# Kernel optimization log

Hardware: AMD Instinct MI355X
Metric: run time of the kernel (lower is better)

Reference implementation:

```python
import jax, jax.numpy as jnp
import numpy as np

NUM_HEADS = 4
EPS = 1e-5


def setup_inputs() -> dict:
    key = jax.random.key(0)
    ks = jax.random.split(key, 5)
    B, C, H, W = 1, 128, 64, 64
    x = jax.random.normal(ks[0], (B, C, H, W), dtype=jnp.float32)
    # 1x1 conv weights [out_c, in_c]; scaled ~ kaiming-ish to keep softmax non-degenerate
    s = 1.0 / np.sqrt(C)
    qw = jax.random.normal(ks[1], (C, C), dtype=jnp.float32) * s
    kw = jax.random.normal(ks[2], (C, C), dtype=jnp.float32) * s
    vw = jax.random.normal(ks[3], (C, C), dtype=jnp.float32) * s
    pw = jax.random.normal(ks[4], (C, C), dtype=jnp.float32) * s
    zeros = jnp.zeros((C,), dtype=jnp.float32)
    return {
        "x": x,
        "gn_w": jnp.ones((C,), dtype=jnp.float32),
        "gn_b": zeros,
        "qw": qw, "qb": zeros,
        "kw": kw, "kb": zeros,
        "vw": vw, "vb": zeros,
        "pw": pw, "pb": zeros,
    }


def reference(x, gn_w, gn_b, qw, qb, kw, kb, vw, vb, pw, pb):
    B, C, H, W = x.shape
    N = H * W
    d = C // NUM_HEADS

    # GroupNorm(num_groups=1): normalize over (C,H,W) per sample, per-channel affine
    mean = jnp.mean(x, axis=(1, 2, 3), keepdims=True)
    var = jnp.var(x, axis=(1, 2, 3), keepdims=True)
    h = (x - mean) * jax.lax.rsqrt(var + EPS)
    h = h * gn_w[None, :, None, None] + gn_b[None, :, None, None]

    hf = h.reshape(B, C, N)  # [B,C,N]

    def conv1x1(w, b):  # 1x1 conv == channel GEMM
        return jnp.einsum('oc,bcn->bon', w, hf) + b[None, :, None]

    q = conv1x1(qw, qb).reshape(B, NUM_HEADS, d, N)
    k = conv1x1(kw, kb).reshape(B, NUM_HEADS, d, N)
    v = conv1x1(vw, vb).reshape(B, NUM_HEADS, d, N)

    scale = d ** (-0.5)
    attn = jnp.einsum('bhdn,bhdm->bhnm', q, k) * scale  # [B,H,N,N]
    attn = jax.nn.softmax(attn, axis=-1)
    out = jnp.einsum('bhnm,bhdm->bhdn', attn, v)  # [B,H,d,N]

    out = out.reshape(B, C, N)
    out = jnp.einsum('oc,bcn->bon', pw, out) + pb[None, :, None]
    return x + out.reshape(B, C, H, W)
```

## Files before the change

kernel.cpp:

```cpp
#include <hip/hip_runtime.h>

#define NPOS 4096
#define NCH  128
#define NTOT (NPOS * NCH)
#define NHEAD 4
#define DH    32
#define NSPLIT 4
#define KSPAN (NPOS / NSPLIT)

typedef __attribute__((ext_vector_type(8))) short short8;
typedef __attribute__((ext_vector_type(4))) float floatx4;
typedef unsigned short u16;
typedef unsigned int   u32;

__device__ __forceinline__ u16 f2bf(float f) {
  u32 u = __float_as_uint(f);
  u += 0x7fffu + ((u >> 16) & 1u);
  return (u16)(u >> 16);
}
__device__ __forceinline__ u32 pack2bf(float a, float b) {
  return (u32)f2bf(a) | ((u32)f2bf(b) << 16);
}
__device__ __forceinline__ u32 pack2bf_fast(float a, float b) {
  return ((__float_as_uint(a) + 0x8000u) >> 16) |
         ((__float_as_uint(b) + 0x8000u) & 0xffff0000u);
}
__device__ __forceinline__ float bf2f(u16 h) {
  return __uint_as_float(((u32)h) << 16);
}

__global__ __launch_bounds__(256) void gn_prep_k(const float* __restrict__ x,
                                                 float2* __restrict__ partials,
                                                 u32* __restrict__ bounds,
                                                 const float* __restrict__ qw, const float* __restrict__ kw,
                                                 const float* __restrict__ vw, const float* __restrict__ pw,
                                                 u16* __restrict__ wq, u16* __restrict__ wk,
                                                 u16* __restrict__ wv, u16* __restrict__ wp) {
  int i = blockIdx.x * 256 + threadIdx.x;
  int w = threadIdx.x >> 6, lane = threadIdx.x & 63;
  float4 a = ((const float4*)x)[i];
  float4 b = ((const float4*)x)[i + 65536];
  float s  = a.x + a.y + a.z + a.w + b.x + b.y + b.z + b.w;
  float sq = a.x*a.x + a.y*a.y + a.z*a.z + a.w*a.w
           + b.x*b.x + b.y*b.y + b.z*b.z + b.w*b.w;
#pragma unroll
  for (int m = 1; m < 64; m <<= 1) {
    s  += __shfl_xor(s, m);
    sq += __shfl_xor(sq, m);
  }
  __shared__ float red[8];
  if (lane == 0) { red[w] = s; red[4 + w] = sq; }
  __syncthreads();
  if (threadIdx.x == 0)
    partials[blockIdx.x] = make_float2(red[0]+red[1]+red[2]+red[3],
                                       red[4]+red[5]+red[6]+red[7]);
  if (blockIdx.x == 0 && threadIdx.x < 4) bounds[threadIdx.x] = 0;
  if (blockIdx.x < 16) {
    int t = blockIdx.x * 256 + threadIdx.x;
    const float sc = 0.17677669529663687f * 1.4426950408889634f;
    float4 v = ((const float4*)qw)[t];
    ((uint2*)wq)[t] = make_uint2(pack2bf(v.x*sc, v.y*sc), pack2bf(v.z*sc, v.w*sc));
    v = ((const float4*)kw)[t];
    ((uint2*)wk)[t] = make_uint2(pack2bf(v.x, v.y), pack2bf(v.z, v.w));
    v = ((const float4*)vw)[t];
    ((uint2*)wv)[t] = make_uint2(pack2bf(v.x, v.y), pack2bf(v.z, v.w));
    v = ((const float4*)pw)[t];
    ((uint2*)wp)[t] = make_uint2(pack2bf(v.x, v.y), pack2bf(v.z, v.w));
  }
}

__global__ __launch_bounds__(256) void qkv_k(const float* __restrict__ x,
    const float* __restrict__ gw, const float* __restrict__ gb,
    const float2* __restrict__ partials,
    const u16* __restrict__ wq, const u16* __restrict__ wk, const u16* __restrict__ wv,
    const float* __restrict__ qb, const float* __restrict__ kb, const float* __restrict__ vb,
    u16* __restrict__ q, u16* __restrict__ k, u16* __restrict__ v, u32* __restrict__ bounds) {
  const int t = threadIdx.x;
  const int w = t >> 6, lane = t & 63;
  const int l16 = lane & 15, quad = lane >> 4;
  const int n0 = blockIdx.x * 16, ow = w * 32;
  const floatx4 zero = {0.f, 0.f, 0.f, 0.f};

  __shared__ float red[8];
  __shared__ float2 swb[128];
  __shared__ __align__(16) u16 hs[16][136];

  float2 p = partials[t];
  float s = p.x, sq = p.y;
#pragma unroll
  for (int m = 1; m < 64; m <<= 1) {
    s  += __shfl_xor(s, m);
    sq += __shfl_xor(sq, m);
  }
  if (lane == 0) { red[w] = s; red[4 + w] = sq; }
  __syncthreads();
  float mean = (red[0]+red[1]+red[2]+red[3]) * (1.0f / NTOT);
  float var  = (red[4]+red[5]+red[6]+red[7]) * (1.0f / NTOT) - mean * mean;
  float rstd = rsqrtf(var + 1e-5f);
  if (t < 128) {
    float swv = gw[t] * rstd;
    swb[t] = make_float2(swv, gb[t] - mean * swv);
  }
  __syncthreads();

#pragma unroll
  for (int i = t; i < 512; i += 256) {
    int c = i >> 2, seg = i & 3;
    float4 xv = *(const float4*)(x + (size_t)c * NPOS + n0 + seg * 4);
    float2 sb = swb[c];
    int nl = seg * 4;
    hs[nl + 0][c] = f2bf(xv.x * sb.x + sb.y);
    hs[nl + 1][c] = f2bf(xv.y * sb.x + sb.y);
    hs[nl + 2][c] = f2bf(xv.z * sb.x + sb.y);
    hs[nl + 3][c] = f2bf(xv.w * sb.x + sb.y);
  }
  __syncthreads();

  short8 bfr[4];
#pragma unroll
  for (int kk = 0; kk < 4; kk++)
    bfr[kk] = *(const short8*)&hs[l16][kk * 32 + quad * 8];

  const int n = n0 + l16;
  {
    floatx4 a0 = zero, a1 = zero;
    const u16* ap = wq + (size_t)(ow + l16) * NCH + quad * 8;
#pragma unroll
    for (int kk = 0; kk < 4; kk++) {
      a0 = __builtin_amdgcn_mfma_f32_16x16x32_bf16(*(const short8*)(ap + kk*32),          bfr[kk], a0, 0,0,0);
      a1 = __builtin_amdgcn_mfma_f32_16x16x32_bf16(*(const short8*)(ap + 16*NCH + kk*32), bfr[kk], a1, 0,0,0);
    }
    const float sc = 0.17677669529663687f * 1.4426950408889634f;
    u16* qp = q + (size_t)(w * NPOS + n) * DH;
#pragma unroll
    for (int ss = 0; ss < 2; ss++) {
      floatx4 acc = ss ? a1 : a0;
      int od = ss * 16 + quad * 4;
      float r0 = acc[0] + qb[ow+od+0]*sc, r1 = acc[1] + qb[ow+od+1]*sc;
      float r2 = acc[2] + qb[ow+od+2]*sc, r3 = acc[3] + qb[ow+od+3]*sc;
      *(uint2*)(qp + od) = make_uint2(pack2bf(r0, r1), pack2bf(r2, r3));
    }
  }
  {
    floatx4 a0 = zero, a1 = zero;
    const u16* ap = wk + (size_t)(ow + l16) * NCH + quad * 8;
#pragma unroll
    for (int kk = 0; kk < 4; kk++) {
      a0 = __builtin_amdgcn_mfma_f32_16x16x32_bf16(*(const short8*)(ap + kk*32),          bfr[kk], a0, 0,0,0);
      a1 = __builtin_amdgcn_mfma_f32_16x16x32_bf16(*(const short8*)(ap + 16*NCH + kk*32), bfr[kk], a1, 0,0,0);
    }
    float sumsq = 0.f;
    u16* kp = k + (size_t)(w * NPOS + n) * DH;
#pragma unroll
    for (int ss = 0; ss < 2; ss++) {
      floatx4 acc = ss ? a1 : a0;
      int od = ss * 16 + quad * 4;
      float r0 = acc[0] + kb[ow+od+0], r1 = acc[1] + kb[ow+od+1];
      float r2 = acc[2] + kb[ow+od+2], r3 = acc[3] + kb[ow+od+3];
      sumsq += r0*r0 + r1*r1 + r2*r2 + r3*r3;
      *(uint2*)(kp + od) = make_uint2(pack2bf(r0, r1), pack2bf(r2, r3));
    }
    sumsq += __shfl_xor(sumsq, 16);
    sumsq += __shfl_xor(sumsq, 32);
#pragma unroll
    for (int m = 1; m < 16; m <<= 1) sumsq = fmaxf(sumsq, __shfl_xor(sumsq, m));
    if (lane == 0) atomicMax(&bounds[w], __float_as_uint(sumsq));
  }
  {
    floatx4 a0 = zero, a1 = zero;
    const u16* ap = wv + (size_t)(ow + l16) * NCH + quad * 8;
#pragma unroll
    for (int kk = 0; kk < 4; kk++) {
      a0 = __builtin_amdgcn_mfma_f32_16x16x32_bf16(*(const short8*)(ap + kk*32),          bfr[kk], a0, 0,0,0);
      a1 = __builtin_amdgcn_mfma_f32_16x16x32_bf16(*(const short8*)(ap + 16*NCH + kk*32), bfr[kk], a1, 0,0,0);
    }
    u16* vp = v + (size_t)(w * DH) * NPOS + n;
#pragma unroll
    for (int ss = 0; ss < 2; ss++) {
      floatx4 acc = ss ? a1 : a0;
      int od = ss * 16 + quad * 4;
#pragma unroll
      for (int r = 0; r < 4; r++)
        vp[(size_t)(od + r) * NPOS] = f2bf(acc[r] + vb[ow + od + r]);
    }
  }
}

__global__ __launch_bounds__(256) void attn_k(const u16* __restrict__ q, const u16* __restrict__ k,
                                              const u16* __restrict__ v, const u32* __restrict__ bounds,
                                              u32* __restrict__ Opair, float* __restrict__ lpart) {
  const int w = threadIdx.x >> 6, lane = threadIdx.x & 63;
  const int l16 = lane & 15, quad = lane >> 4;
  const int s = blockIdx.x >> 8;
  const int q0 = (blockIdx.x & 255) * 16;
  const int head = w;
  __shared__ __align__(16) u16 p_lds[4][2][16][72];

  short8 bq = *(const short8*)(q + (size_t)(head * NPOS + q0 + l16) * DH + quad * 8);
  float qn2 = 0.f;
#pragma unroll
  for (int j = 0; j < 8; j++) { float f = bf2f((u16)bq[j]); qn2 += f * f; }
  qn2 += __shfl_xor(qn2, 16);
  qn2 += __shfl_xor(qn2, 32);
  float kmax = sqrtf(__uint_as_float(bounds[head])) * 1.0005f;
  float bound = sqrtf(qn2) * kmax;

  floatx4 o0 = {0,0,0,0}, o1 = {0,0,0,0}, ol = {0,0,0,0};
  short8 ones;
#pragma unroll
  for (int j = 0; j < 8; j++) ones[j] = (short)0x3F80;

  const u16* kbp = k + (size_t)head * NPOS * DH;
  const u16* vb0 = v + (size_t)(head * DH + l16) * NPOS;
  const u16* vb1 = v + (size_t)(head * DH + 16 + l16) * NPOS;
  const floatx4 zero = {0,0,0,0};
  const int m0beg = s * KSPAN;

#pragma unroll 2
  for (int it = 0; it < KSPAN / 64; it++) {
    const int m0 = m0beg + it * 64;
    const int buf = it & 1;
    floatx4 c[4];
#pragma unroll
    for (int sub = 0; sub < 4; sub++) {
      short8 ak = *(const short8*)(kbp + (size_t)(m0 + sub*16 + l16) * DH + quad * 8);
      c[sub] = __builtin_amdgcn_mfma_f32_16x16x32_bf16(ak, bq, zero, 0, 0, 0);
    }
#pragma unroll
    for (int sub = 0; sub < 4; sub++) {
      float p0 = __builtin_amdgcn_exp2f(c[sub][0] - bound);
      float p1 = __builtin_amdgcn_exp2f(c[sub][1] - bound);
      float p2 = __builtin_amdgcn_exp2f(c[sub][2] - bound);
      float p3 = __builtin_amdgcn_exp2f(c[sub][3] - bound);
      *(uint2*)&p_lds[w][buf][l16][sub * 16 + quad * 4] =
          make_uint2(pack2bf_fast(p0, p1), pack2bf_fast(p2, p3));
    }
#pragma unroll
    for (int kc = 0; kc < 2; kc++) {
      short8 pa  = *(const short8*)&p_lds[w][buf][l16][kc * 32 + quad * 8];
      short8 av0 = *(const short8*)(vb0 + m0 + kc * 32 + quad * 8);
      short8 av1 = *(const short8*)(vb1 + m0 + kc * 32 + quad * 8);
      o0 = __builtin_amdgcn_mfma_f32_16x16x32_bf16(pa, av0, o0, 0, 0, 0);
      o1 = __builtin_amdgcn_mfma_f32_16x16x32_bf16(pa, av1, o1, 0, 0, 0);
      ol = __builtin_amdgcn_mfma_f32_16x16x32_bf16(pa, ones, ol, 0, 0, 0);
    }
  }

  u32*   op = Opair + (size_t)(s * NHEAD + head) * NPOS * 16;
  float* lp = lpart + (size_t)(s * NHEAD + head) * NPOS;
#pragma unroll
  for (int r = 0; r < 4; r++) {
    int qq = q0 + quad * 4 + r;
    op[(size_t)qq * 16 + l16] = pack2bf(o0[r], o1[r]);
    if (l16 == 0) lp[qq] = ol[r];
  }
}

__global__ __launch_bounds__(256) void proj_k(const u32* __restrict__ Opair,
                                              const float* __restrict__ lpart,
                                              const u16* __restrict__ wp,
                                              const float* __restrict__ pb,
                                              const float* __restrict__ x,
                                              float* __restrict__ out) {
  const int w = threadIdx.x >> 6, lane = threadIdx.x & 63;
  const int l16 = lane & 15, quad = lane >> 4;
  const int n0 = blockIdx.x * 16, ow = w * 32;
  const int n = n0 + l16;
  const floatx4 zero = {0.f, 0.f, 0.f, 0.f};
  const bool hi = quad >= 2;

  short8 bfr[4];
#pragma unroll
  for (int kk = 0; kk < 4; kk++) {
    float acc8[8] = {0,0,0,0,0,0,0,0};
    float l = 0.f;
#pragma unroll
    for (int s2 = 0; s2 < NSPLIT; s2++) {
      const u32* pp = Opair + ((size_t)(s2 * NHEAD + kk) * NPOS + n) * 16 + (quad & 1) * 8;
      uint4 u0 = *(const uint4*)pp;
      uint4 u1 = *(const uint4*)(pp + 4);
      u32 uu[8] = {u0.x, u0.y, u0.z, u0.w, u1.x, u1.y, u1.z, u1.w};
#pragma unroll
      for (int j = 0; j < 8; j++)
        acc8[j] += __uint_as_float(hi ? (uu[j] & 0xffff0000u) : (uu[j] << 16));
      l += lpart[(size_t)(s2 * NHEAD + kk) * NPOS + n];
    }
    float inv = 1.0f / fmaxf(l, 1e-30f);
    uint4 u = make_uint4(pack2bf(acc8[0]*inv, acc8[1]*inv),
                         pack2bf(acc8[2]*inv, acc8[3]*inv),
                         pack2bf(acc8[4]*inv, acc8[5]*inv),
                         pack2bf(acc8[6]*inv, acc8[7]*inv));
    bfr[kk] = *(short8*)&u;
  }
  floatx4 a0 = zero, a1 = zero;
  const u16* ap = wp + (size_t)(ow + l16) * NCH + quad * 8;
#pragma unroll
  for (int kk = 0; kk < 4; kk++) {
    a0 = __builtin_amdgcn_mfma_f32_16x16x32_bf16(*(const short8*)(ap + kk*32),          bfr[kk], a0, 0,0,0);
    a1 = __builtin_amdgcn_mfma_f32_16x16x32_bf16(*(const short8*)(ap + 16*NCH + kk*32), bfr[kk], a1, 0,0,0);
  }
#pragma unroll
  for (int ss = 0; ss < 2; ss++) {
    floatx4 acc = ss ? a1 : a0;
    int o = ow + ss * 16 + quad * 4;
#pragma unroll
    for (int r = 0; r < 4; r++) {
      size_t idx = (size_t)(o + r) * NPOS + n;
      out[idx] = acc[r] + pb[o + r] + x[idx];
    }
  }
}

extern "C" void kernel_launch(void* const* d_in, const int* in_sizes, int n_in,
                              void* d_out, int out_size, void* d_ws, size_t ws_size,
                              hipStream_t stream) {
  const float* x   = (const float*)d_in[0];
  const float* gnw = (const float*)d_in[1];
  const float* gnb = (const float*)d_in[2];
  const float* qw  = (const float*)d_in[3];
  const float* qb  = (const float*)d_in[4];
  const float* kw  = (const float*)d_in[5];
  const float* kb  = (const float*)d_in[6];
  const float* vw  = (const float*)d_in[7];
  const float* vb  = (const float*)d_in[8];
  const float* pw  = (const float*)d_in[9];
  const float* pb  = (const float*)d_in[10];
  float* out = (float*)d_out;

  char* wsb = (char*)d_ws;
  float2* partials = (float2*)wsb;
  u32*    bounds   = (u32*)(wsb + 2048);
  u16* wqb = (u16*)(wsb + 4096);
  u16* wkb = wqb + 16384;
  u16* wvb = wkb + 16384;
  u16* wpb = wvb + 16384;
  u16* qbuf = wpb + 16384;
  u16* kbuf = qbuf + NTOT;
  u16* vbuf = kbuf + NTOT;
  u32* Opair = (u32*)(vbuf + NTOT);
  float* lpart = (float*)(Opair + (size_t)NSPLIT * NHEAD * NPOS * 16);

  gn_prep_k<<<256, 256, 0, stream>>>(x, partials, bounds, qw, kw, vw, pw,
                                     wqb, wkb, wvb, wpb);
  qkv_k<<<256, 256, 0, stream>>>(x, gnw, gnb, partials, wqb, wkb, wvb,
                                 qb, kb, vb, qbuf, kbuf, vbuf, bounds);
  attn_k<<<1024, 256, 0, stream>>>(qbuf, kbuf, vbuf, bounds, Opair, lpart);
  proj_k<<<256, 256, 0, stream>>>(Opair, lpart, wpb, pb, x, out);
}
```

Before: 145.6 us.

## Widen per-block parallelism in prep/qkv/proj and register-prefetch K/V in attention

```diff
diff --git a/kernel.cpp b/kernel.cpp
--- a/kernel.cpp
+++ b/kernel.cpp
@@ -7,6 +7,7 @@
 #define DH    32
 #define NSPLIT 4
 #define KSPAN (NPOS / NSPLIT)
+#define NTILE (KSPAN / 64)
 
 typedef __attribute__((ext_vector_type(8))) short short8;
 typedef __attribute__((ext_vector_type(4))) float floatx4;
@@ -39,10 +40,8 @@
   int i = blockIdx.x * 256 + threadIdx.x;
   int w = threadIdx.x >> 6, lane = threadIdx.x & 63;
   float4 a = ((const float4*)x)[i];
-  float4 b = ((const float4*)x)[i + 65536];
-  float s  = a.x + a.y + a.z + a.w + b.x + b.y + b.z + b.w;
-  float sq = a.x*a.x + a.y*a.y + a.z*a.z + a.w*a.w
-           + b.x*b.x + b.y*b.y + b.z*b.z + b.w*b.w;
+  float s  = a.x + a.y + a.z + a.w;
+  float sq = a.x*a.x + a.y*a.y + a.z*a.z + a.w*a.w;
 #pragma unroll
   for (int m = 1; m < 64; m <<= 1) {
     s  += __shfl_xor(s, m);
@@ -69,7 +68,7 @@
   }
 }
 
-__global__ __launch_bounds__(256) void qkv_k(const float* __restrict__ x,
+__global__ __launch_bounds__(768) void qkv_k(const float* __restrict__ x,
     const float* __restrict__ gw, const float* __restrict__ gb,
     const float2* __restrict__ partials,
     const u16* __restrict__ wq, const u16* __restrict__ wk, const u16* __restrict__ wv,
@@ -78,34 +77,35 @@
   const int t = threadIdx.x;
   const int w = t >> 6, lane = t & 63;
   const int l16 = lane & 15, quad = lane >> 4;
-  const int n0 = blockIdx.x * 16, ow = w * 32;
+  const int n0 = blockIdx.x * 16;
   const floatx4 zero = {0.f, 0.f, 0.f, 0.f};
 
-  __shared__ float red[8];
+  __shared__ float red[16];
   __shared__ float2 swb[128];
   __shared__ __align__(16) u16 hs[16][136];
 
-  float2 p = partials[t];
-  float s = p.x, sq = p.y;
-#pragma unroll
-  for (int m = 1; m < 64; m <<= 1) {
-    s  += __shfl_xor(s, m);
-    sq += __shfl_xor(sq, m);
-  }
-  if (lane == 0) { red[w] = s; red[4 + w] = sq; }
-  __syncthreads();
-  float mean = (red[0]+red[1]+red[2]+red[3]) * (1.0f / NTOT);
-  float var  = (red[4]+red[5]+red[6]+red[7]) * (1.0f / NTOT) - mean * mean;
+  if (t < 512) {
+    float2 p = partials[t];
+    float s = p.x, sq = p.y;
+#pragma unroll
+    for (int m = 1; m < 64; m <<= 1) {
+      s  += __shfl_xor(s, m);
+      sq += __shfl_xor(sq, m);
+    }
+    if (lane == 0) { red[w] = s; red[8 + w] = sq; }
+  }
+  __syncthreads();
+  float mean = (red[0]+red[1]+red[2]+red[3]+red[4]+red[5]+red[6]+red[7]) * (1.0f / NTOT);
+  float var  = (red[8]+red[9]+red[10]+red[11]+red[12]+red[13]+red[14]+red[15]) * (1.0f / NTOT)
+               - mean * mean;
   float rstd = rsqrtf(var + 1e-5f);
   if (t < 128) {
     float swv = gw[t] * rstd;
     swb[t] = make_float2(swv, gb[t] - mean * swv);
   }
   __syncthreads();
-
-#pragma unroll
-  for (int i = t; i < 512; i += 256) {
-    int c = i >> 2, seg = i & 3;
+  if (t < 512) {
+    int c = t >> 2, seg = t & 3;
     float4 xv = *(const float4*)(x + (size_t)c * NPOS + n0 + seg * 4);
     float2 sb = swb[c];
     int nl = seg * 4;
@@ -121,17 +121,19 @@
   for (int kk = 0; kk < 4; kk++)
     bfr[kk] = *(const short8*)&hs[l16][kk * 32 + quad * 8];
 
+  const int mat = w >> 2, head = w & 3, ow = head * 32;
+  const u16* wm = (mat == 0) ? wq : (mat == 1) ? wk : wv;
+  floatx4 a0 = zero, a1 = zero;
+  const u16* ap = wm + (size_t)(ow + l16) * NCH + quad * 8;
+#pragma unroll
+  for (int kk = 0; kk < 4; kk++) {
+    a0 = __builtin_amdgcn_mfma_f32_16x16x32_bf16(*(const short8*)(ap + kk*32),          bfr[kk], a0, 0,0,0);
+    a1 = __builtin_amdgcn_mfma_f32_16x16x32_bf16(*(const short8*)(ap + 16*NCH + kk*32), bfr[kk], a1, 0,0,0);
+  }
   const int n = n0 + l16;
-  {
-    floatx4 a0 = zero, a1 = zero;
-    const u16* ap = wq + (size_t)(ow + l16) * NCH + quad * 8;
-#pragma unroll
-    for (int kk = 0; kk < 4; kk++) {
-      a0 = __builtin_amdgcn_mfma_f32_16x16x32_bf16(*(const short8*)(ap + kk*32),          bfr[kk], a0, 0,0,0);
-      a1 = __builtin_amdgcn_mfma_f32_16x16x32_bf16(*(const short8*)(ap + 16*NCH + kk*32), bfr[kk], a1, 0,0,0);
-    }
+  if (mat == 0) {
     const float sc = 0.17677669529663687f * 1.4426950408889634f;
-    u16* qp = q + (size_t)(w * NPOS + n) * DH;
+    u16* qp = q + (size_t)(head * NPOS + n) * DH;
 #pragma unroll
     for (int ss = 0; ss < 2; ss++) {
       floatx4 acc = ss ? a1 : a0;
@@ -140,17 +142,9 @@
       float r2 = acc[2] + qb[ow+od+2]*sc, r3 = acc[3] + qb[ow+od+3]*sc;
       *(uint2*)(qp + od) = make_uint2(pack2bf(r0, r1), pack2bf(r2, r3));
     }
-  }
-  {
-    floatx4 a0 = zero, a1 = zero;
-    const u16* ap = wk + (size_t)(ow + l16) * NCH + quad * 8;
-#pragma unroll
-    for (int kk = 0; kk < 4; kk++) {
-      a0 = __builtin_amdgcn_mfma_f32_16x16x32_bf16(*(const short8*)(ap + kk*32),          bfr[kk], a0, 0,0,0);
-      a1 = __builtin_amdgcn_mfma_f32_16x16x32_bf16(*(const short8*)(ap + 16*NCH + kk*32), bfr[kk], a1, 0,0,0);
-    }
+  } else if (mat == 1) {
     float sumsq = 0.f;
-    u16* kp = k + (size_t)(w * NPOS + n) * DH;
+    u16* kp = k + (size_t)(head * NPOS + n) * DH;
 #pragma unroll
     for (int ss = 0; ss < 2; ss++) {
       floatx4 acc = ss ? a1 : a0;
@@ -164,17 +158,9 @@
     sumsq += __shfl_xor(sumsq, 32);
 #pragma unroll
     for (int m = 1; m < 16; m <<= 1) sumsq = fmaxf(sumsq, __shfl_xor(sumsq, m));
-    if (lane == 0) atomicMax(&bounds[w], __float_as_uint(sumsq));
-  }
-  {
-    floatx4 a0 = zero, a1 = zero;
-    const u16* ap = wv + (size_t)(ow + l16) * NCH + quad * 8;
-#pragma unroll
-    for (int kk = 0; kk < 4; kk++) {
-      a0 = __builtin_amdgcn_mfma_f32_16x16x32_bf16(*(const short8*)(ap + kk*32),          bfr[kk], a0, 0,0,0);
-      a1 = __builtin_amdgcn_mfma_f32_16x16x32_bf16(*(const short8*)(ap + 16*NCH + kk*32), bfr[kk], a1, 0,0,0);
-    }
-    u16* vp = v + (size_t)(w * DH) * NPOS + n;
+    if (lane == 0) atomicMax(&bounds[head], __float_as_uint(sumsq));
+  } else {
+    u16* vp = v + (size_t)(head * DH) * NPOS + n;
 #pragma unroll
     for (int ss = 0; ss < 2; ss++) {
       floatx4 acc = ss ? a1 : a0;
@@ -210,22 +196,41 @@
 #pragma unroll
   for (int j = 0; j < 8; j++) ones[j] = (short)0x3F80;
 
-  const u16* kbp = k + (size_t)head * NPOS * DH;
-  const u16* vb0 = v + (size_t)(head * DH + l16) * NPOS;
-  const u16* vb1 = v + (size_t)(head * DH + 16 + l16) * NPOS;
+  const u16* kbp = k + (size_t)head * NPOS * DH + quad * 8;
+  const u16* vb0 = v + (size_t)(head * DH + l16) * NPOS + quad * 8;
+  const u16* vb1 = vb0 + (size_t)16 * NPOS;
   const floatx4 zero = {0,0,0,0};
-  const int m0beg = s * KSPAN;
-
-#pragma unroll 2
-  for (int it = 0; it < KSPAN / 64; it++) {
-    const int m0 = m0beg + it * 64;
+
+  int m0 = s * KSPAN;
+  short8 ak[4], av[4];
+#pragma unroll
+  for (int sub = 0; sub < 4; sub++)
+    ak[sub] = *(const short8*)(kbp + (size_t)(m0 + sub * 16 + l16) * DH);
+#pragma unroll
+  for (int kc = 0; kc < 2; kc++) {
+    av[2*kc]   = *(const short8*)(vb0 + m0 + kc * 32);
+    av[2*kc+1] = *(const short8*)(vb1 + m0 + kc * 32);
+  }
+
+  for (int it = 0; it < NTILE; it++) {
+    const int mn = m0 + 64;
+    const bool more = (it + 1 < NTILE);
+    short8 nak[4], nav[4];
+    if (more) {
+#pragma unroll
+      for (int sub = 0; sub < 4; sub++)
+        nak[sub] = *(const short8*)(kbp + (size_t)(mn + sub * 16 + l16) * DH);
+#pragma unroll
+      for (int kc = 0; kc < 2; kc++) {
+        nav[2*kc]   = *(const short8*)(vb0 + mn + kc * 32);
+        nav[2*kc+1] = *(const short8*)(vb1 + mn + kc * 32);
+      }
+    }
     const int buf = it & 1;
     floatx4 c[4];
 #pragma unroll
-    for (int sub = 0; sub < 4; sub++) {
-      short8 ak = *(const short8*)(kbp + (size_t)(m0 + sub*16 + l16) * DH + quad * 8);
-      c[sub] = __builtin_amdgcn_mfma_f32_16x16x32_bf16(ak, bq, zero, 0, 0, 0);
-    }
+    for (int sub = 0; sub < 4; sub++)
+      c[sub] = __builtin_amdgcn_mfma_f32_16x16x32_bf16(ak[sub], bq, zero, 0, 0, 0);
 #pragma unroll
     for (int sub = 0; sub < 4; sub++) {
       float p0 = __builtin_amdgcn_exp2f(c[sub][0] - bound);
@@ -237,13 +242,16 @@
     }
 #pragma unroll
     for (int kc = 0; kc < 2; kc++) {
-      short8 pa  = *(const short8*)&p_lds[w][buf][l16][kc * 32 + quad * 8];
-      short8 av0 = *(const short8*)(vb0 + m0 + kc * 32 + quad * 8);
-      short8 av1 = *(const short8*)(vb1 + m0 + kc * 32 + quad * 8);
-      o0 = __builtin_amdgcn_mfma_f32_16x16x32_bf16(pa, av0, o0, 0, 0, 0);
-      o1 = __builtin_amdgcn_mfma_f32_16x16x32_bf16(pa, av1, o1, 0, 0, 0);
-      ol = __builtin_amdgcn_mfma_f32_16x16x32_bf16(pa, ones, ol, 0, 0, 0);
-    }
+      short8 pa = *(const short8*)&p_lds[w][buf][l16][kc * 32 + quad * 8];
+      o0 = __builtin_amdgcn_mfma_f32_16x16x32_bf16(pa, av[2*kc],   o0, 0, 0, 0);
+      o1 = __builtin_amdgcn_mfma_f32_16x16x32_bf16(pa, av[2*kc+1], o1, 0, 0, 0);
+      ol = __builtin_amdgcn_mfma_f32_16x16x32_bf16(pa, ones,       ol, 0, 0, 0);
+    }
+    if (more) {
+#pragma unroll
+      for (int j = 0; j < 4; j++) { ak[j] = nak[j]; av[j] = nav[j]; }
+    }
+    m0 = mn;
   }
 
   u32*   op = Opair + (size_t)(s * NHEAD + head) * NPOS * 16;
@@ -256,58 +264,58 @@
   }
 }
 
-__global__ __launch_bounds__(256) void proj_k(const u32* __restrict__ Opair,
+__global__ __launch_bounds__(512) void proj_k(const u32* __restrict__ Opair,
                                               const float* __restrict__ lpart,
                                               const u16* __restrict__ wp,
                                               const float* __restrict__ pb,
                                               const float* __restrict__ x,
                                               float* __restrict__ out) {
-  const int w = threadIdx.x >> 6, lane = threadIdx.x & 63;
+  const int t = threadIdx.x;
+  const int w = t >> 6, lane = t & 63;
   const int l16 = lane & 15, quad = lane >> 4;
-  const int n0 = blockIdx.x * 16, ow = w * 32;
+  const int n0 = blockIdx.x * 16;
+  const floatx4 zero = {0.f, 0.f, 0.f, 0.f};
+  __shared__ __align__(16) u16 at_lds[16][136];
+
+  {
+    const int n = t & 15, ci = t >> 4;
+    const int c0 = ci * 4, head = c0 >> 5, off = c0 & 31;
+    const int half = off >> 4, j0 = off & 15;
+    float acc[4] = {0.f, 0.f, 0.f, 0.f};
+    float l = 0.f;
+#pragma unroll
+    for (int s2 = 0; s2 < NSPLIT; s2++) {
+      const u32* pp = Opair + ((size_t)(s2 * NHEAD + head) * NPOS + n0 + n) * 16 + j0;
+      uint4 u = *(const uint4*)pp;
+      u32 uu[4] = {u.x, u.y, u.z, u.w};
+#pragma unroll
+      for (int j = 0; j < 4; j++)
+        acc[j] += half ? __uint_as_float(uu[j] & 0xffff0000u)
+                       : __uint_as_float(uu[j] << 16);
+      l += lpart[(size_t)(s2 * NHEAD + head) * NPOS + n0 + n];
+    }
+    float inv = 1.0f / fmaxf(l, 1e-30f);
+    *(uint2*)&at_lds[n][c0] = make_uint2(pack2bf(acc[0]*inv, acc[1]*inv),
+                                         pack2bf(acc[2]*inv, acc[3]*inv));
+  }
+  __syncthreads();
+
+  short8 bfr[4];
+#pragma unroll
+  for (int kk = 0; kk < 4; kk++)
+    bfr[kk] = *(const short8*)&at_lds[l16][kk * 32 + quad * 8];
+  const int ow = w * 16;
+  floatx4 a0 = zero;
+  const u16* ap = wp + (size_t)(ow + l16) * NCH + quad * 8;
+#pragma unroll
+  for (int kk = 0; kk < 4; kk++)
+    a0 = __builtin_amdgcn_mfma_f32_16x16x32_bf16(*(const short8*)(ap + kk*32), bfr[kk], a0, 0,0,0);
   const int n = n0 + l16;
-  const floatx4 zero = {0.f, 0.f, 0.f, 0.f};
-  const bool hi = quad >= 2;
-
-  short8 bfr[4];
-#pragma unroll
-  for (int kk = 0; kk < 4; kk++) {
-    float acc8[8] = {0,0,0,0,0,0,0,0};
-    float l = 0.f;
-#pragma unroll
-    for (int s2 = 0; s2 < NSPLIT; s2++) {
-      const u32* pp = Opair + ((size_t)(s2 * NHEAD + kk) * NPOS + n) * 16 + (quad & 1) * 8;
-      uint4 u0 = *(const uint4*)pp;
-      uint4 u1 = *(const uint4*)(pp + 4);
-      u32 uu[8] = {u0.x, u0.y, u0.z, u0.w, u1.x, u1.y, u1.z, u1.w};
-#pragma unroll
-      for (int j = 0; j < 8; j++)
-        acc8[j] += __uint_as_float(hi ? (uu[j] & 0xffff0000u) : (uu[j] << 16));
-      l += lpart[(size_t)(s2 * NHEAD + kk) * NPOS + n];
-    }
-    float inv = 1.0f / fmaxf(l, 1e-30f);
-    uint4 u = make_uint4(pack2bf(acc8[0]*inv, acc8[1]*inv),
-                         pack2bf(acc8[2]*inv, acc8[3]*inv),
-                         pack2bf(acc8[4]*inv, acc8[5]*inv),
-                         pack2bf(acc8[6]*inv, acc8[7]*inv));
-    bfr[kk] = *(short8*)&u;
-  }
-  floatx4 a0 = zero, a1 = zero;
-  const u16* ap = wp + (size_t)(ow + l16) * NCH + quad * 8;
-#pragma unroll
-  for (int kk = 0; kk < 4; kk++) {
-    a0 = __builtin_amdgcn_mfma_f32_16x16x32_bf16(*(const short8*)(ap + kk*32),          bfr[kk], a0, 0,0,0);
-    a1 = __builtin_amdgcn_mfma_f32_16x16x32_bf16(*(const short8*)(ap + 16*NCH + kk*32), bfr[kk], a1, 0,0,0);
-  }
-#pragma unroll
-  for (int ss = 0; ss < 2; ss++) {
-    floatx4 acc = ss ? a1 : a0;
-    int o = ow + ss * 16 + quad * 4;
-#pragma unroll
-    for (int r = 0; r < 4; r++) {
-      size_t idx = (size_t)(o + r) * NPOS + n;
-      out[idx] = acc[r] + pb[o + r] + x[idx];
-    }
+#pragma unroll
+  for (int r = 0; r < 4; r++) {
+    int o = ow + quad * 4 + r;
+    size_t idx = (size_t)o * NPOS + n;
+    out[idx] = a0[r] + pb[o] + x[idx];
   }
 }
 
@@ -329,8 +337,8 @@
 
   char* wsb = (char*)d_ws;
   float2* partials = (float2*)wsb;
-  u32*    bounds   = (u32*)(wsb + 2048);
-  u16* wqb = (u16*)(wsb + 4096);
+  u32*    bounds   = (u32*)(wsb + 4096);
+  u16* wqb = (u16*)(wsb + 8192);
   u16* wkb = wqb + 16384;
   u16* wvb = wkb + 16384;
   u16* wpb = wvb + 16384;
@@ -340,10 +348,10 @@
   u32* Opair = (u32*)(vbuf + NTOT);
   float* lpart = (float*)(Opair + (size_t)NSPLIT * NHEAD * NPOS * 16);
 
-  gn_prep_k<<<256, 256, 0, stream>>>(x, partials, bounds, qw, kw, vw, pw,
+  gn_prep_k<<<512, 256, 0, stream>>>(x, partials, bounds, qw, kw, vw, pw,
                                      wqb, wkb, wvb, wpb);
-  qkv_k<<<256, 256, 0, stream>>>(x, gnw, gnb, partials, wqb, wkb, wvb,
+  qkv_k<<<256, 768, 0, stream>>>(x, gnw, gnb, partials, wqb, wkb, wvb,
                                  qb, kb, vb, qbuf, kbuf, vbuf, bounds);
-  attn_k<<<1024, 256, 0, stream>>>(qbuf, kbuf, vbuf, bounds, Opair, lpart);
-  proj_k<<<256, 256, 0, stream>>>(Opair, lpart, wpb, pb, x, out);
-}
+  attn_k<<<256 * NSPLIT, 256, 0, stream>>>(qbuf, kbuf, vbuf, bounds, Opair, lpart);
+  proj_k<<<256, 512, 0, stream>>>(Opair, lpart, wpb, pb, x, out);
+}
```

Measured after the change: 144.5 us. No clear change (-0.8%).
